# Performance work log

Measured on AMD Instinct MI355X. Metric: run time of the kernel, lower is better.

The kernel has to match this reference:

```python
import jax, jax.numpy as jnp
import numpy as np

NSIDE = 64
NLAT = 4 * NSIDE - 1        # 255 iso-latitude rings
NLON = 4 * NSIDE            # 256 = max pixels per ring
NPIX = 12 * NSIDE * NSIDE   # 49152 HEALPix pixels
LMAX = NLAT                 # 255
MMAX = NLON // 2 + 1        # 129
BATCH, CHAN = 8, 32


def _ring_geometry():
    # HEALPix ring scheme: ring r (0-based), 1-based i=r+1
    #  north cap i<nside: nph=4i, phi shift 0.5
    #  equatorial nside<=i<=3*nside: nph=4*nside, shift alternates {0,0.5}
    #  south cap: mirror of north cap
    nph = np.zeros(NLAT, np.int64)
    shift = np.zeros(NLAT, np.float64)
    for r in range(NLAT):
        i = r + 1
        if i < NSIDE:
            nph[r], shift[r] = 4 * i, 0.5
        elif i <= 3 * NSIDE:
            nph[r], shift[r] = 4 * NSIDE, 0.5 * ((i - NSIDE + 1) % 2)
        else:
            nph[r], shift[r] = 4 * (NLAT - r), 0.5
    offs = np.concatenate([[0], np.cumsum(nph)[:-1]])
    p = np.arange(NLON)
    mask = (p[None, :] < nph[:, None])                       # [nlat, nlon]
    idx = (offs[:, None] + p[None, :]) * mask                # padded -> 0
    phase = 2.0 * np.pi * (p[None, :] + shift[:, None]) / nph[:, None] * mask
    return idx.astype(np.int32), mask.astype(np.float32), phase.astype(np.float32)


def setup_inputs() -> dict:
    key = jax.random.key(0)
    k1, k2, k3 = jax.random.split(key, 3)
    idx, mask, phase = _ring_geometry()
    x = jax.random.normal(k1, (BATCH, CHAN, NPIX), jnp.float32)
    pct = jax.random.normal(k2, (MMAX, LMAX, NLAT), jnp.float32) * 0.1  # Legendre table stand-in
    w = jax.random.uniform(k3, (NLAT,), jnp.float32)                    # per-ring quadrature weights
    return {"x": x, "pct": pct, "w": w,
            "ring_index": jnp.asarray(idx),
            "ring_mask": jnp.asarray(mask),
            "phase": jnp.asarray(phase)}


def _healpix_rfft_real(x, ring_index, ring_mask, phase):
    # x: [..., npix] -> per-ring DFT coefficients as real pairs [..., nlat, mmax, 2]
    rings = x[..., ring_index] * ring_mask                 # [..., nlat, nlon]
    m = jnp.arange(MMAX, dtype=phase.dtype)
    ang = phase[:, :, None] * m                            # [nlat, nlon, mmax]
    fr = jnp.einsum('...kp,kpm->...km', rings, jnp.cos(ang))
    fi = -jnp.einsum('...kp,kpm->...km', rings, jnp.sin(ang))
    return jnp.stack([fr, fi], axis=-1)                    # n=2 is view_as_real axis


def reference(x, pct, w, ring_index, ring_mask, phase):
    # healpix ring rFFT, then Legendre contraction (einsum '...kmn,mlk->...lmn')
    f = _healpix_rfft_real(x, ring_index, ring_mask, phase)  # [..., nlat, mmax, 2]
    weights = pct * w                                        # [mmax, lmax, nlat]
    out = jnp.einsum('...kmn,mlk->...lmn', f, weights)       # [..., lmax, mmax, 2]
    return out
```

## Files before the change

### kernel.cpp

```cpp
#include <hip/hip_runtime.h>

#define NLAT 255
#define NLON 256
#define NPIX 49152
#define MMAX 129
#define MCS  258
#define NTBL 65
#define TROWS 264

typedef unsigned short ushort_t;
typedef __attribute__((ext_vector_type(8)))  short  bf16x8;
typedef __attribute__((ext_vector_type(4)))  short  short4v;
typedef __attribute__((ext_vector_type(16))) float  f32x16;
typedef __attribute__((ext_vector_type(4)))  float  float4v;
typedef __attribute__((ext_vector_type(4), aligned(4))) float float4u;

__device__ __forceinline__ ushort_t f2bf(float f) {
    union { float f; unsigned u; } v; v.f = f;
    unsigned r = v.u + 0x7FFFu + ((v.u >> 16) & 1u);
    return (ushort_t)(r >> 16);
}
__device__ __forceinline__ float bf2f(ushort_t h) {
    union { unsigned u; float f; } v; v.u = ((unsigned)h) << 16;
    return v.f;
}

__global__ __launch_bounds__(256) void trigK(const float* __restrict__ phase,
                                             const float* __restrict__ mask,
                                             ushort_t* __restrict__ Ttab2) {
    const int tt  = blockIdx.x;
    const int mcs = blockIdx.y;
    const int p   = threadIdx.x;
    const int r   = (tt < 63) ? tt : (tt == 63 ? 63 : 64);
    float val = 0.f;
    if (mcs < MCS) {
        float ph = phase[r * NLON + p];
        float mk = mask[r * NLON + p];
        float fm = (float)(mcs >> 1);
        float s, c;
        __sincosf(ph * fm, &s, &c);
        val = (mcs & 1) ? (-s * mk) : (c * mk);
    }
    Ttab2[(((size_t)tt * 4 + (p >> 6)) * TROWS + mcs) * 64 + (p & 63)] = f2bf(val);
}

__global__ __launch_bounds__(512, 2) void stageA(const float* __restrict__ x,
                                                 const int* __restrict__ ring_index,
                                                 const ushort_t* __restrict__ Ttab2,
                                                 ushort_t* __restrict__ f1) {
    __shared__ __align__(16) ushort_t Rs[256 * 72];
    __shared__ __align__(16) ushort_t Ts[TROWS * 72];

    const int r  = blockIdx.x;
    const int i1 = r + 1;
    const int nph = (i1 < 64) ? 4 * i1 : (i1 <= 192 ? 256 : 4 * (256 - i1));
    const int tbl = (i1 < 64) ? r : (i1 <= 192 ? (63 + (((i1 - 63) & 1) ^ 1)) : 254 - r);
    const int base = ring_index[r * NLON];

    const int t    = threadIdx.x;
    const int lane = t & 63;
    const int wid  = t >> 6;
    const int wrow = wid >> 1, wcol = wid & 1;
    const int lg   = lane >> 5;
    const int lc   = lane & 31;

    f32x16 acc[5][2];
#pragma unroll
    for (int tau = 0; tau < 5; ++tau)
#pragma unroll
        for (int i = 0; i < 2; ++i)
#pragma unroll
            for (int q = 0; q < 16; ++q) acc[tau][i][q] = 0.f;

    for (int pc = 0; pc < nph; pc += 64) {
        {
            const int p0 = (t & 15) * 4;
            const bool ok = (pc + p0) < nph;
#pragma unroll
            for (int pass = 0; pass < 8; ++pass) {
                int bc = (t >> 4) + pass * 32;
                float4v v = {0.f, 0.f, 0.f, 0.f};
                if (ok) v = *(const float4v*)(x + (size_t)bc * NPIX + base + pc + p0);
                short4v h;
                h[0] = (short)f2bf(v[0]); h[1] = (short)f2bf(v[1]);
                h[2] = (short)f2bf(v[2]); h[3] = (short)f2bf(v[3]);
                *(short4v*)(Rs + bc * 72 + p0) = h;
            }
        }
        {
            const ushort_t* slab = Ttab2 + ((size_t)tbl * 4 + (pc >> 6)) * (TROWS * 64);
#pragma unroll
            for (int pass = 0; pass < 5; ++pass) {
                int id = t + pass * 512;
                if (id < (TROWS * 64 / 8)) {
                    bf16x8 v = *(const bf16x8*)(slab + id * 8);
                    *(bf16x8*)(Ts + (id >> 3) * 72 + (id & 7) * 8) = v;
                }
            }
        }
        __syncthreads();
#pragma unroll
        for (int ks = 0; ks < 4; ++ks) {
            bf16x8 a0 = *(const bf16x8*)(Rs + (wrow * 64 + lc) * 72 + ks * 16 + lg * 8);
            bf16x8 a1 = *(const bf16x8*)(Rs + (wrow * 64 + 32 + lc) * 72 + ks * 16 + lg * 8);
#pragma unroll
            for (int tau = 0; tau < 5; ++tau) {
                int rr = tau * 64 + wcol * 32 + lc;
                int trow = rr > (TROWS - 1) ? (TROWS - 1) : rr;
                bf16x8 b = *(const bf16x8*)(Ts + trow * 72 + ks * 16 + lg * 8);
                acc[tau][0] = __builtin_amdgcn_mfma_f32_32x32x16_bf16(a0, b, acc[tau][0], 0, 0, 0);
                acc[tau][1] = __builtin_amdgcn_mfma_f32_32x32x16_bf16(a1, b, acc[tau][1], 0, 0, 0);
            }
        }
        __syncthreads();
    }

    ushort_t* Olds = Rs;
#pragma unroll
    for (int tau = 0; tau < 5; ++tau) {
        __syncthreads();
        {
            const int mcsl = wcol * 32 + lc;
#pragma unroll
            for (int i = 0; i < 2; ++i)
#pragma unroll
                for (int q = 0; q < 16; ++q) {
                    int bc = wrow * 64 + i * 32 + 4 * lg + (q & 3) + 8 * (q >> 2);
                    Olds[mcsl * 264 + bc] = f2bf(acc[tau][i][q]);
                }
        }
        __syncthreads();
#pragma unroll
        for (int it = 0; it < 4; ++it) {
            int row = (t >> 5) + it * 16;
            int ch  = t & 31;
            int mcs = tau * 64 + row;
            if (mcs < MCS) {
                bf16x8 v = *(const bf16x8*)(Olds + row * 264 + ch * 8);
                int m = mcs >> 1, n = mcs & 1;
                *(bf16x8*)(f1 + ((size_t)m * NLAT + r) * 512 + n * 256 + ch * 8) = v;
            }
        }
    }
}

__global__ __launch_bounds__(256) void transK(const ushort_t* __restrict__ f1,
                                              ushort_t* __restrict__ f1t, int m0) {
    __shared__ __align__(16) ushort_t T[64][72];
    const int m  = m0 + blockIdx.x;
    const int k0 = blockIdx.y * 64;
    const int b0 = blockIdx.z * 64;
    const int t  = threadIdx.x;
#pragma unroll
    for (int it = 0; it < 2; ++it) {
        int id = t + it * 256;
        int kk = id >> 3, ch = id & 7;
        int k  = k0 + kk;
        bf16x8 v = {0,0,0,0,0,0,0,0};
        if (k < NLAT)
            v = *(const bf16x8*)(f1 + ((size_t)m * NLAT + k) * 512 + b0 + ch * 8);
        *(bf16x8*)(&T[kk][ch * 8]) = v;
    }
    __syncthreads();
#pragma unroll
    for (int it = 0; it < 2; ++it) {
        int id  = t + it * 256;
        int bb  = id & 63, ch8 = id >> 6;
        bf16x8 v;
#pragma unroll
        for (int j = 0; j < 8; ++j) v[j] = T[ch8 * 8 + j][bb];
        *(bf16x8*)(f1t + ((size_t)m * 512 + b0 + bb) * 256 + k0 + ch8 * 8) = v;
    }
}

__global__ __launch_bounds__(256, 2) void stageB(const ushort_t* __restrict__ f1t,
                                                 const float* __restrict__ pct,
                                                 const float* __restrict__ w,
                                                 ushort_t* __restrict__ otmp,
                                                 int mbase) {
    __shared__ __align__(16) ushort_t SB[30720];
    ushort_t* As = SB;
    ushort_t* Ws = SB + 10240;
    ushort_t* Es = SB;

    int m, sub;
    if (mbase == 0) { m = blockIdx.x >> 2; sub = blockIdx.x & 3; }
    else {
        int mm = ((blockIdx.x >> 5) << 3) | (blockIdx.x & 7);
        if (mm > 126) return;
        m = mbase + mm;
        sub = (blockIdx.x >> 3) & 3;
    }
    const int b2t = sub * 128;

    const int t     = threadIdx.x;
    const int lane  = t & 63;
    const int wid   = t >> 6;
    const int wrow  = wid >> 1, wlcol = wid & 1;
    const int lg    = lane >> 5, lc = lane & 31;

    f32x16 acc[2][4];
#pragma unroll
    for (int i = 0; i < 2; ++i)
#pragma unroll
        for (int j = 0; j < 4; ++j)
#pragma unroll
            for (int q = 0; q < 16; ++q) acc[i][j][q] = 0.f;

    auto fillA = [&](ushort_t* dst, int kc) {
#pragma unroll
        for (int pass = 0; pass < 2; ++pass) {
            int id  = t + pass * 256;
            int row = id >> 2, ch = id & 3;
            bf16x8 v = *(const bf16x8*)(f1t + ((size_t)m * 512 + b2t + row) * 256 + kc + ch * 8);
            *(bf16x8*)(dst + row * 40 + ch * 8) = v;
        }
    };
    auto fillW = [&](ushort_t* dst, int kc) {
#pragma unroll
        for (int pass = 0; pass < 2; ++pass) {
            int id   = t + pass * 256;
            int lrow = id >> 1, half = id & 1;
            int kb   = kc + half * 16;
            float vals[16];
            if (lrow < NLAT) {
                const float* src = pct + ((size_t)m * NLAT + lrow) * NLAT + kb;
#pragma unroll
                for (int c = 0; c < 4; ++c) {
                    int k4 = kb + c * 4;
                    if (k4 + 4 <= NLAT) {
                        float4u pv = *(const float4u*)(src + c * 4);
                        float4v wv = *(const float4v*)(w + k4);
#pragma unroll
                        for (int j = 0; j < 4; ++j) vals[c * 4 + j] = pv[j] * wv[j];
                    } else {
#pragma unroll
                        for (int j = 0; j < 4; ++j) {
                            int k = k4 + j;
                            vals[c * 4 + j] = (k < NLAT) ? src[c * 4 + j] * w[k] : 0.f;
                        }
                    }
                }
            } else {
#pragma unroll
                for (int c = 0; c < 16; ++c) vals[c] = 0.f;
            }
            ushort_t* d = dst + lrow * 40 + half * 16;
#pragma unroll
            for (int c = 0; c < 4; ++c) {
                short4v h;
                h[0] = (short)f2bf(vals[c * 4 + 0]);
                h[1] = (short)f2bf(vals[c * 4 + 1]);
                h[2] = (short)f2bf(vals[c * 4 + 2]);
                h[3] = (short)f2bf(vals[c * 4 + 3]);
                *(short4v*)(d + c * 4) = h;
            }
        }
    };

    fillA(As, 0);
    fillW(Ws, 0);
    __syncthreads();
    int buf = 0;
    for (int kc = 0; kc < 256; kc += 32, buf ^= 1) {
        if (kc + 32 < 256) {
            fillA(As + (buf ^ 1) * 5120, kc + 32);
            fillW(Ws + (buf ^ 1) * 10240, kc + 32);
        }
        const ushort_t* A = As + buf * 5120;
        const ushort_t* W = Ws + buf * 10240;
#pragma unroll
        for (int ks = 0; ks < 2; ++ks) {
            const int ko = ks * 16 + lg * 8;
            bf16x8 a0 = *(const bf16x8*)(A + (wrow * 64 + lc) * 40 + ko);
            bf16x8 a1 = *(const bf16x8*)(A + (wrow * 64 + 32 + lc) * 40 + ko);
#pragma unroll
            for (int jj = 0; jj < 4; ++jj) {
                bf16x8 b = *(const bf16x8*)(W + (wlcol * 128 + jj * 32 + lc) * 40 + ko);
                acc[0][jj] = __builtin_amdgcn_mfma_f32_32x32x16_bf16(a0, b, acc[0][jj], 0, 0, 0);
                acc[1][jj] = __builtin_amdgcn_mfma_f32_32x32x16_bf16(a1, b, acc[1][jj], 0, 0, 0);
            }
        }
        __syncthreads();
    }

#pragma unroll
    for (int h = 0; h < 2; ++h) {
        if (h) __syncthreads();
        if (wlcol == h) {
#pragma unroll
            for (int i = 0; i < 2; ++i)
#pragma unroll
                for (int jj = 0; jj < 4; ++jj)
#pragma unroll
                    for (int q = 0; q < 16; ++q) {
                        int bl = wrow * 64 + i * 32 + 4 * lg + (q & 3) + 8 * (q >> 2);
                        Es[bl * 136 + jj * 32 + lc] = f2bf(acc[i][jj][q]);
                    }
        }
        __syncthreads();
#pragma unroll
        for (int it = 0; it < 8; ++it) {
            int id  = t + it * 256;
            int row = id >> 4, ch = id & 15;
            bf16x8 v = *(const bf16x8*)(Es + row * 136 + ch * 8);
            *(bf16x8*)(otmp + (((size_t)m * 512 + b2t + row) << 8) + h * 128 + ch * 8) = v;
        }
    }
}

__global__ __launch_bounds__(256) void permuteK(const ushort_t* __restrict__ otmp,
                                                float* __restrict__ out) {
    __shared__ ushort_t L[MCS * 66];
    const int bc = blockIdx.x;
    const int l0 = blockIdx.y * 64;
    const int t  = threadIdx.x;
    const int ll = t & 63;
    const int l  = l0 + ll;
#pragma unroll 4
    for (int it = 0; it < 65; ++it) {
        int mn = (t >> 6) + it * 4;
        if (mn < MCS) {
            int mm = mn >> 1, n = mn & 1;
            ushort_t v = 0;
            if (l < NLAT)
                v = otmp[(((size_t)mm * 512 + n * 256 + bc) << 8) + l];
            L[mn * 66 + ll] = v;
        }
    }
    __syncthreads();
    for (int ll2 = 0; ll2 < 64; ++ll2) {
        int lo = l0 + ll2;
        if (lo >= NLAT) break;
        size_t rowb = ((size_t)bc * NLAT + lo) * MCS;
        out[rowb + t] = bf2f(L[t * 66 + ll2]);
        if (t < 2)
            out[rowb + 256 + t] = bf2f(L[(256 + t) * 66 + ll2]);
    }
}

extern "C" void kernel_launch(void* const* d_in, const int* in_sizes, int n_in,
                              void* d_out, int out_size, void* d_ws, size_t ws_size,
                              hipStream_t stream) {
    const float* x          = (const float*)d_in[0];
    const float* pct        = (const float*)d_in[1];
    const float* w          = (const float*)d_in[2];
    const int*   ring_index = (const int*)d_in[3];
    const float* ring_mask  = (const float*)d_in[4];
    const float* phase      = (const float*)d_in[5];
    float* out = (float*)d_out;

    char* wsb = (char*)d_ws;
    ushort_t* f1    = (ushort_t*)wsb;
    ushort_t* Ttab2 = (ushort_t*)(wsb + 33684480);
    ushort_t* f1t   = (ushort_t*)(wsb + 33552384);
    ushort_t* otmp  = (ushort_t*)wsb;

    trigK   <<<dim3(NTBL, TROWS), 256, 0, stream>>>(phase, ring_mask, Ttab2);
    stageA  <<<dim3(NLAT),      512, 0, stream>>>(x, ring_index, Ttab2, f1);
    transK  <<<dim3(1, 4, 8),   256, 0, stream>>>(f1, f1t, 128);
    transK  <<<dim3(128, 4, 8), 256, 0, stream>>>(f1, f1t, 0);
    stageB  <<<dim3(8),         256, 0, stream>>>(f1t, pct, w, otmp, 0);
    stageB  <<<dim3(544),       256, 0, stream>>>(f1t, pct, w, otmp, 2);
    permuteK<<<dim3(256, 4),    256, 0, stream>>>(otmp, out);
}
```

Baseline: 137.8 us.

## Precompute bf16 weighted Legendre table in a prep kernel; simplify stageB tiling

A new prepK kernel multiplies pct by the ring weights once, converts to bf16 and stores a padded 256x256-per-m table in the output buffer as scratch. stageB then loads this table with aligned 16-byte vector copies instead of doing unaligned fp32 loads, multiplies and conversions inside its K loop, which halves the bytes it reads for weights. The stageB launch split also changes from 8+544 blocks with remapped indices to 256+260 blocks with a plain m/sub mapping. The cost is an extra kernel that reads all of pct and writes about 17 MB of bf16 scratch, plus reliance on the output buffer being free until permuteK runs.

New measurement: 142.4 us. +3.4%, slower.

```diff
diff --git a/kernel.cpp b/kernel.cpp
--- a/kernel.cpp
+++ b/kernel.cpp
@@ -13,7 +13,6 @@
 typedef __attribute__((ext_vector_type(4)))  short  short4v;
 typedef __attribute__((ext_vector_type(16))) float  f32x16;
 typedef __attribute__((ext_vector_type(4)))  float  float4v;
-typedef __attribute__((ext_vector_type(4), aligned(4))) float float4u;
 
 __device__ __forceinline__ ushort_t f2bf(float f) {
     union { float f; unsigned u; } v; v.f = f;
@@ -23,6 +22,21 @@
 __device__ __forceinline__ float bf2f(ushort_t h) {
     union { unsigned u; float f; } v; v.u = ((unsigned)h) << 16;
     return v.f;
+}
+
+__global__ __launch_bounds__(256) void prepK(const float* __restrict__ pct,
+                                             const float* __restrict__ w,
+                                             ushort_t* __restrict__ pctw) {
+    const int m  = blockIdx.x;
+    const int l0 = blockIdx.y * 32;
+    const int t  = threadIdx.x;
+    const float wk = (t < NLAT) ? w[t] : 0.f;
+    for (int l = l0; l < l0 + 32; ++l) {
+        float v = 0.f;
+        if (l < NLAT && t < NLAT)
+            v = pct[((size_t)m * NLAT + l) * NLAT + t] * wk;
+        pctw[((size_t)m * 256 + l) * 256 + t] = f2bf(v);
+    }
 }
 
 __global__ __launch_bounds__(256) void trigK(const float* __restrict__ phase,
@@ -174,8 +188,7 @@
 }
 
 __global__ __launch_bounds__(256, 2) void stageB(const ushort_t* __restrict__ f1t,
-                                                 const float* __restrict__ pct,
-                                                 const float* __restrict__ w,
+                                                 const ushort_t* __restrict__ pctw,
                                                  ushort_t* __restrict__ otmp,
                                                  int mbase) {
     __shared__ __align__(16) ushort_t SB[30720];
@@ -183,14 +196,8 @@
     ushort_t* Ws = SB + 10240;
     ushort_t* Es = SB;
 
-    int m, sub;
-    if (mbase == 0) { m = blockIdx.x >> 2; sub = blockIdx.x & 3; }
-    else {
-        int mm = ((blockIdx.x >> 5) << 3) | (blockIdx.x & 7);
-        if (mm > 126) return;
-        m = mbase + mm;
-        sub = (blockIdx.x >> 3) & 3;
-    }
+    const int m   = mbase + (blockIdx.x >> 2);
+    const int sub = blockIdx.x & 3;
     const int b2t = sub * 128;
 
     const int t     = threadIdx.x;
@@ -218,43 +225,11 @@
     };
     auto fillW = [&](ushort_t* dst, int kc) {
 #pragma unroll
-        for (int pass = 0; pass < 2; ++pass) {
-            int id   = t + pass * 256;
-            int lrow = id >> 1, half = id & 1;
-            int kb   = kc + half * 16;
-            float vals[16];
-            if (lrow < NLAT) {
-                const float* src = pct + ((size_t)m * NLAT + lrow) * NLAT + kb;
-#pragma unroll
-                for (int c = 0; c < 4; ++c) {
-                    int k4 = kb + c * 4;
-                    if (k4 + 4 <= NLAT) {
-                        float4u pv = *(const float4u*)(src + c * 4);
-                        float4v wv = *(const float4v*)(w + k4);
-#pragma unroll
-                        for (int j = 0; j < 4; ++j) vals[c * 4 + j] = pv[j] * wv[j];
-                    } else {
-#pragma unroll
-                        for (int j = 0; j < 4; ++j) {
-                            int k = k4 + j;
-                            vals[c * 4 + j] = (k < NLAT) ? src[c * 4 + j] * w[k] : 0.f;
-                        }
-                    }
-                }
-            } else {
-#pragma unroll
-                for (int c = 0; c < 16; ++c) vals[c] = 0.f;
-            }
-            ushort_t* d = dst + lrow * 40 + half * 16;
-#pragma unroll
-            for (int c = 0; c < 4; ++c) {
-                short4v h;
-                h[0] = (short)f2bf(vals[c * 4 + 0]);
-                h[1] = (short)f2bf(vals[c * 4 + 1]);
-                h[2] = (short)f2bf(vals[c * 4 + 2]);
-                h[3] = (short)f2bf(vals[c * 4 + 3]);
-                *(short4v*)(d + c * 4) = h;
-            }
+        for (int pass = 0; pass < 4; ++pass) {
+            int id  = t + pass * 256;
+            int row = id >> 2, ch = id & 3;
+            bf16x8 v = *(const bf16x8*)(pctw + ((size_t)m * 256 + row) * 256 + kc + ch * 8);
+            *(bf16x8*)(dst + row * 40 + ch * 8) = v;
         }
     };
 
@@ -355,12 +330,14 @@
     ushort_t* Ttab2 = (ushort_t*)(wsb + 33684480);
     ushort_t* f1t   = (ushort_t*)(wsb + 33552384);
     ushort_t* otmp  = (ushort_t*)wsb;
-
+    ushort_t* pctw  = (ushort_t*)d_out;
+
+    prepK   <<<dim3(MMAX, 8),   256, 0, stream>>>(pct, w, pctw);
     trigK   <<<dim3(NTBL, TROWS), 256, 0, stream>>>(phase, ring_mask, Ttab2);
     stageA  <<<dim3(NLAT),      512, 0, stream>>>(x, ring_index, Ttab2, f1);
     transK  <<<dim3(1, 4, 8),   256, 0, stream>>>(f1, f1t, 128);
     transK  <<<dim3(128, 4, 8), 256, 0, stream>>>(f1, f1t, 0);
-    stageB  <<<dim3(8),         256, 0, stream>>>(f1t, pct, w, otmp, 0);
-    stageB  <<<dim3(544),       256, 0, stream>>>(f1t, pct, w, otmp, 2);
+    stageB  <<<dim3(256),       256, 0, stream>>>(f1t, pctw, otmp, 0);
+    stageB  <<<dim3(260),       256, 0, stream>>>(f1t, pctw, otmp, 64);
     permuteK<<<dim3(256, 4),    256, 0, stream>>>(otmp, out);
 }
```
